# Performance work log

Measured on AMD Instinct MI355X. Metric: run time of the kernel, lower is better.

Reference implementation:

```python
import jax, jax.numpy as jnp
import numpy as np

MOMENTUM = 0.9
SHRINK = 0.0025
EPS_ATTN = 1e-8
EPS_NORM = 1e-12


def setup_inputs() -> dict:
    key = jax.random.key(0)
    ks = jax.random.split(key, 6)
    N, L, C, M = 64, 2048, 256, 128
    query = jax.random.normal(ks[0], (N, L, C), dtype=jnp.float32)
    mem = jax.random.normal(ks[1], (M, C), dtype=jnp.float32)
    # mimic xavier_normal + L2 row-normalize init
    mem = mem * np.sqrt(2.0 / (M + C))
    mem = mem / jnp.maximum(jnp.linalg.norm(mem, axis=1, keepdims=True), EPS_NORM)
    scale = 1.0 / np.sqrt(C)
    U_w = jax.random.uniform(ks[2], (C, C), jnp.float32, -scale, scale)
    U_b = jax.random.uniform(ks[3], (C,), jnp.float32, -scale, scale)
    W_w = jax.random.uniform(ks[4], (C, C), jnp.float32, -scale, scale)
    W_b = jax.random.uniform(ks[5], (C,), jnp.float32, -scale, scale)
    return {"query": query, "mem": mem, "U_w": U_w, "U_b": U_b, "W_w": W_w, "W_b": W_b}


def _hard_shrink_relu(x, lambd=SHRINK, epsilon=EPS_NORM):
    d = x - lambd
    return jax.nn.relu(d) * x / (jnp.abs(d) + epsilon)


def reference(query, mem, U_w, U_b, W_w, W_b):
    N, L, C = query.shape
    M = mem.shape[0]
    q = query.reshape(-1, C)  # T x C

    # ---- update (torch.no_grad block) ----
    qd = jax.lax.stop_gradient(q)
    m = jax.lax.stop_gradient(mem)
    attn_u = jax.nn.softmax(qd @ m.T, axis=-1)          # T x M
    attn_u = jnp.maximum(attn_u, EPS_ATTN)
    add_mem = attn_u.T @ qd                              # M x C
    gate = jax.nn.sigmoid(m @ U_w.T + U_b + add_mem @ W_w.T + W_b)
    new_mem = MOMENTUM * m + (1.0 - MOMENTUM) * ((1.0 - gate) * m + gate * add_mem)
    new_mem = new_mem / jnp.maximum(jnp.linalg.norm(new_mem, axis=1, keepdims=True), EPS_NORM)
    new_mem = jax.lax.stop_gradient(new_mem)

    # ---- read (memory detached, query differentiable) ----
    attn = jax.nn.softmax(q @ new_mem.T, axis=-1)        # T x M
    attn = _hard_shrink_relu(attn)
    attn = attn / jnp.maximum(jnp.sum(jnp.abs(attn), axis=1, keepdims=True), EPS_NORM)
    add_memory = attn @ new_mem                          # T x C
    out = jnp.concatenate([q, add_memory], axis=1)       # T x 2C

    out = out.reshape(N, L, 2 * C)
    attn = attn.reshape(N, L, M)
    return out, attn, new_mem
```

## Files before the change

### kernel.cpp

```cpp
#include <hip/hip_runtime.h>
#include <hip/hip_bf16.h>

#define T_TOT 131072

typedef __bf16 v8bf __attribute__((ext_vector_type(8)));
typedef float  v4f  __attribute__((ext_vector_type(4)));

#define MFMA16(a, b, c) __builtin_amdgcn_mfma_f32_16x16x32_bf16(a, b, c, 0, 0, 0)

__device__ __forceinline__ unsigned short f2bf(float x) {
  unsigned int u = __float_as_uint(x);
  u += 0x7fffu + ((u >> 16) & 1u);
  return (unsigned short)(u >> 16);
}
__device__ __forceinline__ ushort4 f2bf4(float4 v) {
  ushort4 r; r.x = f2bf(v.x); r.y = f2bf(v.y); r.z = f2bf(v.z); r.w = f2bf(v.w);
  return r;
}

__global__ void prep_kernel(const float* __restrict__ mem,
                            unsigned short* __restrict__ memb,
                            float* __restrict__ add_mem) {
  int i = blockIdx.x * 256 + threadIdx.x;
  memb[i] = f2bf(mem[i]);
  add_mem[i] = 0.f;
}

template <bool IS_READ>
__global__ __launch_bounds__(256, 2)
void attn_kernel(const float* __restrict__ q,
                 const unsigned short* __restrict__ memb,
                 unsigned short* __restrict__ attnT,
                 unsigned short* __restrict__ qbT,
                 float* __restrict__ attn_out,
                 const unsigned short* __restrict__ nmT,
                 float* __restrict__ out) {
  constexpr int R1 = 33792;
  __shared__ __align__(16) char smem[IS_READ ? (R1 + 17408) : R1];
  unsigned short* qs   = (unsigned short*)smem;
  unsigned short* ms   = (unsigned short*)(smem + 9216);
  float*          S    = (float*)smem;
  unsigned short* nmTl = (unsigned short*)smem;
  unsigned short* P    = (unsigned short*)(smem + R1);

  const int tid  = threadIdx.x;
  const int wave = tid >> 6, lane = tid & 63, l15 = lane & 15, quad = lane >> 4;
  const int t0 = blockIdx.x * 64;
  const int rh = wave >> 1, mh = wave & 1;

  v4f acc[2][4] = {};

  for (int kc = 0; kc < 256; kc += 64) {
    __syncthreads();
#pragma unroll
    for (int i = 0; i < 4; ++i) {
      int f4 = tid + i * 256, row = f4 >> 4, c4 = f4 & 15;
      float4 v = *(const float4*)(q + (size_t)(t0 + row) * 256 + kc + c4 * 4);
      if constexpr (IS_READ)
        *(float4*)(out + (size_t)(t0 + row) * 512 + kc + c4 * 4) = v;
      *(ushort4*)(qs + row * 72 + c4 * 4) = f2bf4(v);
    }
#pragma unroll
    for (int i = 0; i < 4; ++i) {
      int g = tid + i * 256, m = g >> 3, c8 = g & 7;
      *(uint4*)(ms + m * 72 + c8 * 8) = *(const uint4*)(memb + m * 256 + kc + c8 * 8);
    }
    __syncthreads();
#pragma unroll
    for (int s = 0; s < 2; ++s) {
      int ko = s * 32 + quad * 8;
      v8bf a0 = *(const v8bf*)(qs + (rh * 32 + l15) * 72 + ko);
      v8bf a1 = *(const v8bf*)(qs + (rh * 32 + 16 + l15) * 72 + ko);
#pragma unroll
      for (int j = 0; j < 4; ++j) {
        v8bf b = *(const v8bf*)(ms + (mh * 64 + j * 16 + l15) * 72 + ko);
        acc[0][j] = MFMA16(a0, b, acc[0][j]);
        acc[1][j] = MFMA16(a1, b, acc[1][j]);
      }
    }
    if constexpr (!IS_READ) {
      int c4 = tid & 63, g = tid >> 6;
      const unsigned short* qcol = qs + c4;
      unsigned int pk2[8];
#pragma unroll
      for (int j = 0; j < 8; ++j) {
        unsigned int lo = qcol[(g * 16 + j * 2) * 72];
        unsigned int hi = qcol[(g * 16 + j * 2 + 1) * 72];
        pk2[j] = lo | (hi << 16);
      }
      uint4* dq = (uint4*)(qbT + (size_t)(kc + c4) * T_TOT + t0 + g * 16);
      dq[0] = make_uint4(pk2[0], pk2[1], pk2[2], pk2[3]);
      dq[1] = make_uint4(pk2[4], pk2[5], pk2[6], pk2[7]);
    }
  }
  __syncthreads();
#pragma unroll
  for (int i = 0; i < 2; ++i)
#pragma unroll
    for (int j = 0; j < 4; ++j)
#pragma unroll
      for (int r = 0; r < 4; ++r)
        S[(rh * 32 + i * 16 + quad * 4 + r) * 132 + mh * 64 + j * 16 + l15] = acc[i][j][r];
  __syncthreads();

  const int row = tid >> 2, p = tid & 3;
  float4 v[8];
  float mx = -1e30f;
#pragma unroll
  for (int k = 0; k < 8; ++k) {
    v[k] = *(const float4*)(S + row * 132 + p * 32 + k * 4);
    mx = fmaxf(mx, fmaxf(fmaxf(v[k].x, v[k].y), fmaxf(v[k].z, v[k].w)));
  }
  mx = fmaxf(mx, __shfl_xor(mx, 1, 64));
  mx = fmaxf(mx, __shfl_xor(mx, 2, 64));
  float sum = 0.f;
#pragma unroll
  for (int k = 0; k < 8; ++k) {
    v[k].x = __expf(v[k].x - mx); v[k].y = __expf(v[k].y - mx);
    v[k].z = __expf(v[k].z - mx); v[k].w = __expf(v[k].w - mx);
    sum += v[k].x + v[k].y + v[k].z + v[k].w;
  }
  sum += __shfl_xor(sum, 1, 64);
  sum += __shfl_xor(sum, 2, 64);
  float inv = 1.f / sum;

  if constexpr (!IS_READ) {
#pragma unroll
    for (int k = 0; k < 8; ++k) {
      v[k].x = fmaxf(v[k].x * inv, 1e-8f); v[k].y = fmaxf(v[k].y * inv, 1e-8f);
      v[k].z = fmaxf(v[k].z * inv, 1e-8f); v[k].w = fmaxf(v[k].w * inv, 1e-8f);
      *(float4*)(S + row * 132 + p * 32 + k * 4) = v[k];
    }
    __syncthreads();
    int m = tid >> 1, hf = tid & 1;
    unsigned int pk[16];
#pragma unroll
    for (int k2 = 0; k2 < 16; ++k2) {
      unsigned int lo = f2bf(S[(hf * 32 + k2 * 2) * 132 + m]);
      unsigned int hi = f2bf(S[(hf * 32 + k2 * 2 + 1) * 132 + m]);
      pk[k2] = lo | (hi << 16);
    }
    uint4* dst = (uint4*)(attnT + (size_t)m * T_TOT + t0 + hf * 32);
    dst[0] = make_uint4(pk[0], pk[1], pk[2], pk[3]);
    dst[1] = make_uint4(pk[4], pk[5], pk[6], pk[7]);
    dst[2] = make_uint4(pk[8], pk[9], pk[10], pk[11]);
    dst[3] = make_uint4(pk[12], pk[13], pk[14], pk[15]);
  } else {
    float ysum = 0.f;
#pragma unroll
    for (int k = 0; k < 8; ++k) {
      float* e = (float*)&v[k];
#pragma unroll
      for (int c = 0; c < 4; ++c) {
        float a2 = e[c] * inv;
        float dd = a2 - 0.0025f;
        float y  = dd > 0.f ? a2 * dd / (dd + 1e-12f) : 0.f;
        e[c] = y; ysum += y;
      }
    }
    ysum += __shfl_xor(ysum, 1, 64);
    ysum += __shfl_xor(ysum, 2, 64);
    float dn = 1.f / fmaxf(ysum, 1e-12f);
#pragma unroll
    for (int k = 0; k < 8; ++k) {
      float4 w; w.x = v[k].x * dn; w.y = v[k].y * dn; w.z = v[k].z * dn; w.w = v[k].w * dn;
      *(float4*)(attn_out + (size_t)(t0 + row) * 128 + p * 32 + k * 4) = w;
      *(ushort4*)(P + row * 136 + p * 32 + k * 4) = f2bf4(w);
    }
    __syncthreads();

    v4f acc2[16] = {};
    for (int mc = 0; mc < 128; mc += 32) {
#pragma unroll
      for (int i = 0; i < 4; ++i) {
        int g = tid + i * 256, cr = g >> 2, c8 = g & 3;
        *(uint4*)(nmTl + cr * 56 + c8 * 8) = *(const uint4*)(nmT + cr * 128 + mc + c8 * 8);
      }
      __syncthreads();
      v8bf af = *(const v8bf*)(P + (wave * 16 + l15) * 136 + mc + quad * 8);
#pragma unroll
      for (int j2 = 0; j2 < 16; ++j2) {
        v8bf bf = *(const v8bf*)(nmTl + (j2 * 16 + l15) * 56 + quad * 8);
        acc2[j2] = MFMA16(af, bf, acc2[j2]);
      }
      __syncthreads();
    }
#pragma unroll
    for (int j2 = 0; j2 < 16; ++j2)
#pragma unroll
      for (int r = 0; r < 4; ++r)
        out[(size_t)(t0 + wave * 16 + quad * 4 + r) * 512 + 256 + j2 * 16 + l15] = acc2[j2][r];
  }
}

__global__ __launch_bounds__(256, 2)
void addmem_kernel(const unsigned short* __restrict__ attnT,
                   const unsigned short* __restrict__ qbT,
                   float* __restrict__ add_mem) {
  __shared__ __align__(16) char smem[36864];
  unsigned short* at_l = (unsigned short*)smem;
  unsigned short* qb_l = (unsigned short*)(smem + 18432);
  const int tid  = threadIdx.x;
  const int wave = tid >> 6, lane = tid & 63, l15 = lane & 15, quad = lane >> 4;
  const int h  = blockIdx.x & 1;
  const int tc = blockIdx.x >> 1;
  const int wm = wave & 1, wc = wave >> 1;
  v4f acc[4][4] = {};

  for (int kk = 0; kk < 8; ++kk) {
    int kb = tc * 512 + kk * 64;
    __syncthreads();
#pragma unroll
    for (int i = 0; i < 4; ++i) {
      int g = tid + i * 256, m = g >> 3, t8 = g & 7;
      *(uint4*)(at_l + m * 72 + t8 * 8) =
          *(const uint4*)(attnT + (size_t)m * T_TOT + kb + t8 * 8);
      *(uint4*)(qb_l + m * 72 + t8 * 8) =
          *(const uint4*)(qbT + (size_t)(h * 128 + m) * T_TOT + kb + t8 * 8);
    }
    __syncthreads();
#pragma unroll
    for (int s = 0; s < 2; ++s) {
      int ko = s * 32 + quad * 8;
      v8bf a[4], b[4];
#pragma unroll
      for (int jm = 0; jm < 4; ++jm)
        a[jm] = *(const v8bf*)(at_l + (wm * 64 + jm * 16 + l15) * 72 + ko);
#pragma unroll
      for (int jc = 0; jc < 4; ++jc)
        b[jc] = *(const v8bf*)(qb_l + (wc * 64 + jc * 16 + l15) * 72 + ko);
#pragma unroll
      for (int jm = 0; jm < 4; ++jm)
#pragma unroll
        for (int jc = 0; jc < 4; ++jc)
          acc[jm][jc] = MFMA16(a[jm], b[jc], acc[jm][jc]);
    }
  }
#pragma unroll
  for (int jm = 0; jm < 4; ++jm)
#pragma unroll
    for (int jc = 0; jc < 4; ++jc)
#pragma unroll
      for (int r = 0; r < 4; ++r)
        atomicAdd(add_mem + (wm * 64 + jm * 16 + quad * 4 + r) * 256 +
                      h * 128 + wc * 64 + jc * 16 + l15,
                  acc[jm][jc][r]);
}

__global__ __launch_bounds__(256)
void update_kernel(const float* __restrict__ mem, const float* __restrict__ add_mem,
                   const float* __restrict__ U_w, const float* __restrict__ U_b,
                   const float* __restrict__ W_w, const float* __restrict__ W_b,
                   float* __restrict__ nm_out, unsigned short* __restrict__ nm_bf,
                   unsigned short* __restrict__ nmT_bf) {
  const int m = blockIdx.x, c = threadIdx.x;
  __shared__ float mrow[256], arow[256], red[8];
  mrow[c] = mem[m * 256 + c];
  arow[c] = add_mem[m * 256 + c];
  __syncthreads();
  float g = U_b[c] + W_b[c];
  const float4* uw = (const float4*)(U_w + (size_t)c * 256);
  const float4* ww = (const float4*)(W_w + (size_t)c * 256);
#pragma unroll 8
  for (int k = 0; k < 64; ++k) {
    float4 u4 = uw[k], w4 = ww[k];
    g += u4.x * mrow[k * 4] + u4.y * mrow[k * 4 + 1] + u4.z * mrow[k * 4 + 2] + u4.w * mrow[k * 4 + 3];
    g += w4.x * arow[k * 4] + w4.y * arow[k * 4 + 1] + w4.z * arow[k * 4 + 2] + w4.w * arow[k * 4 + 3];
  }
  float gate = 1.f / (1.f + __expf(-g));
  float nmv = mrow[c] * (1.f - 0.1f * gate) + 0.1f * gate * arow[c];
  float ss = nmv * nmv;
#pragma unroll
  for (int o = 1; o < 64; o <<= 1) ss += __shfl_xor(ss, o, 64);
  int wv = c >> 6, lane = c & 63;
  if (lane == 0) red[wv] = ss;
  __syncthreads();
  if (c == 0) red[4] = 1.f / fmaxf(sqrtf(red[0] + red[1] + red[2] + red[3]), 1e-12f);
  __syncthreads();
  float nv = nmv * red[4];
  nm_out[m * 256 + c] = nv;
  unsigned short b = f2bf(nv);
  nm_bf[m * 256 + c] = b;
  nmT_bf[c * 128 + m] = b;
}

extern "C" void kernel_launch(void* const* d_in, const int* in_sizes, int n_in,
                              void* d_out, int out_size, void* d_ws, size_t ws_size,
                              hipStream_t stream) {
  (void)in_sizes; (void)n_in; (void)out_size; (void)ws_size;
  const float* q   = (const float*)d_in[0];
  const float* mem = (const float*)d_in[1];
  const float* U_w = (const float*)d_in[2];
  const float* U_b = (const float*)d_in[3];
  const float* W_w = (const float*)d_in[4];
  const float* W_b = (const float*)d_in[5];

  float* out      = (float*)d_out;
  float* attn_out = out + (size_t)T_TOT * 512;
  float* nm_out   = attn_out + (size_t)T_TOT * 128;

  float*          add_mem = (float*)d_ws;
  unsigned short* mem_bf  = (unsigned short*)((char*)d_ws + 131072);
  unsigned short* nm_bf   = (unsigned short*)((char*)d_ws + 196608);
  unsigned short* nmT_bf  = (unsigned short*)((char*)d_ws + 262144);
  unsigned short* attnT = (unsigned short*)attn_out;
  unsigned short* qbT   = (unsigned short*)out;

  prep_kernel<<<128, 256, 0, stream>>>(mem, mem_bf, add_mem);
  attn_kernel<false><<<2048, 256, 0, stream>>>(q, mem_bf, attnT, qbT, nullptr, nullptr, nullptr);
  addmem_kernel<<<512, 256, 0, stream>>>(attnT, qbT, add_mem);
  update_kernel<<<128, 256, 0, stream>>>(mem, add_mem, U_w, U_b, W_w, W_b,
                                         nm_out, nm_bf, nmT_bf);
  attn_kernel<true><<<2048, 256, 0, stream>>>(q, nm_bf, nullptr, nullptr, attn_out, nmT_bf, out);
}
```

Measured before the change: 569.7 us.

## Split attention kernel and load read-pass operands directly from global memory

The templated attention kernel is split into separate write and read kernels. The read kernel no longer stages query and memory tiles in LDS. Each lane loads its query fragment straight from global memory, converts it to bf16 in registers, and reads memory and the transposed new-memory B fragments directly from global (cache-resident) instead of through shared memory. This removes several __syncthreads and LDS round trips. In exchange it issues more redundant global/L2 loads per wave and uses less-coalesced access patterns.

```diff
diff --git a/kernel.cpp b/kernel.cpp
--- a/kernel.cpp
+++ b/kernel.cpp
@@ -16,6 +16,11 @@
 __device__ __forceinline__ ushort4 f2bf4(float4 v) {
   ushort4 r; r.x = f2bf(v.x); r.y = f2bf(v.y); r.z = f2bf(v.z); r.w = f2bf(v.w);
   return r;
+}
+__device__ __forceinline__ v8bf f2bf8(float4 lo, float4 hi) {
+  union { ushort4 u[2]; v8bf v; } r;
+  r.u[0] = f2bf4(lo); r.u[1] = f2bf4(hi);
+  return r.v;
 }
 
 __global__ void prep_kernel(const float* __restrict__ mem,
@@ -26,22 +31,15 @@
   add_mem[i] = 0.f;
 }
 
-template <bool IS_READ>
 __global__ __launch_bounds__(256, 2)
-void attn_kernel(const float* __restrict__ q,
-                 const unsigned short* __restrict__ memb,
-                 unsigned short* __restrict__ attnT,
-                 unsigned short* __restrict__ qbT,
-                 float* __restrict__ attn_out,
-                 const unsigned short* __restrict__ nmT,
-                 float* __restrict__ out) {
-  constexpr int R1 = 33792;
-  __shared__ __align__(16) char smem[IS_READ ? (R1 + 17408) : R1];
-  unsigned short* qs   = (unsigned short*)smem;
-  unsigned short* ms   = (unsigned short*)(smem + 9216);
-  float*          S    = (float*)smem;
-  unsigned short* nmTl = (unsigned short*)smem;
-  unsigned short* P    = (unsigned short*)(smem + R1);
+void attn_write_kernel(const float* __restrict__ q,
+                       const unsigned short* __restrict__ memb,
+                       unsigned short* __restrict__ attnT,
+                       unsigned short* __restrict__ qbT) {
+  __shared__ __align__(16) char smem[33792];
+  unsigned short* qs = (unsigned short*)smem;
+  unsigned short* ms = (unsigned short*)(smem + 9216);
+  float*          S  = (float*)smem;
 
   const int tid  = threadIdx.x;
   const int wave = tid >> 6, lane = tid & 63, l15 = lane & 15, quad = lane >> 4;
@@ -56,8 +54,6 @@
     for (int i = 0; i < 4; ++i) {
       int f4 = tid + i * 256, row = f4 >> 4, c4 = f4 & 15;
       float4 v = *(const float4*)(q + (size_t)(t0 + row) * 256 + kc + c4 * 4);
-      if constexpr (IS_READ)
-        *(float4*)(out + (size_t)(t0 + row) * 512 + kc + c4 * 4) = v;
       *(ushort4*)(qs + row * 72 + c4 * 4) = f2bf4(v);
     }
 #pragma unroll
@@ -78,7 +74,7 @@
         acc[1][j] = MFMA16(a1, b, acc[1][j]);
       }
     }
-    if constexpr (!IS_READ) {
+    {
       int c4 = tid & 63, g = tid >> 6;
       const unsigned short* qcol = qs + c4;
       unsigned int pk2[8];
@@ -124,73 +120,135 @@
   sum += __shfl_xor(sum, 2, 64);
   float inv = 1.f / sum;
 
-  if constexpr (!IS_READ) {
-#pragma unroll
-    for (int k = 0; k < 8; ++k) {
-      v[k].x = fmaxf(v[k].x * inv, 1e-8f); v[k].y = fmaxf(v[k].y * inv, 1e-8f);
-      v[k].z = fmaxf(v[k].z * inv, 1e-8f); v[k].w = fmaxf(v[k].w * inv, 1e-8f);
-      *(float4*)(S + row * 132 + p * 32 + k * 4) = v[k];
-    }
-    __syncthreads();
-    int m = tid >> 1, hf = tid & 1;
-    unsigned int pk[16];
-#pragma unroll
-    for (int k2 = 0; k2 < 16; ++k2) {
-      unsigned int lo = f2bf(S[(hf * 32 + k2 * 2) * 132 + m]);
-      unsigned int hi = f2bf(S[(hf * 32 + k2 * 2 + 1) * 132 + m]);
-      pk[k2] = lo | (hi << 16);
-    }
-    uint4* dst = (uint4*)(attnT + (size_t)m * T_TOT + t0 + hf * 32);
-    dst[0] = make_uint4(pk[0], pk[1], pk[2], pk[3]);
-    dst[1] = make_uint4(pk[4], pk[5], pk[6], pk[7]);
-    dst[2] = make_uint4(pk[8], pk[9], pk[10], pk[11]);
-    dst[3] = make_uint4(pk[12], pk[13], pk[14], pk[15]);
-  } else {
-    float ysum = 0.f;
-#pragma unroll
-    for (int k = 0; k < 8; ++k) {
-      float* e = (float*)&v[k];
-#pragma unroll
-      for (int c = 0; c < 4; ++c) {
-        float a2 = e[c] * inv;
-        float dd = a2 - 0.0025f;
-        float y  = dd > 0.f ? a2 * dd / (dd + 1e-12f) : 0.f;
-        e[c] = y; ysum += y;
-      }
-    }
-    ysum += __shfl_xor(ysum, 1, 64);
-    ysum += __shfl_xor(ysum, 2, 64);
-    float dn = 1.f / fmaxf(ysum, 1e-12f);
-#pragma unroll
-    for (int k = 0; k < 8; ++k) {
-      float4 w; w.x = v[k].x * dn; w.y = v[k].y * dn; w.z = v[k].z * dn; w.w = v[k].w * dn;
-      *(float4*)(attn_out + (size_t)(t0 + row) * 128 + p * 32 + k * 4) = w;
-      *(ushort4*)(P + row * 136 + p * 32 + k * 4) = f2bf4(w);
-    }
-    __syncthreads();
-
-    v4f acc2[16] = {};
-    for (int mc = 0; mc < 128; mc += 32) {
-#pragma unroll
-      for (int i = 0; i < 4; ++i) {
-        int g = tid + i * 256, cr = g >> 2, c8 = g & 3;
-        *(uint4*)(nmTl + cr * 56 + c8 * 8) = *(const uint4*)(nmT + cr * 128 + mc + c8 * 8);
-      }
-      __syncthreads();
-      v8bf af = *(const v8bf*)(P + (wave * 16 + l15) * 136 + mc + quad * 8);
-#pragma unroll
-      for (int j2 = 0; j2 < 16; ++j2) {
-        v8bf bf = *(const v8bf*)(nmTl + (j2 * 16 + l15) * 56 + quad * 8);
-        acc2[j2] = MFMA16(af, bf, acc2[j2]);
-      }
-      __syncthreads();
-    }
-#pragma unroll
-    for (int j2 = 0; j2 < 16; ++j2)
+#pragma unroll
+  for (int k = 0; k < 8; ++k) {
+    v[k].x = fmaxf(v[k].x * inv, 1e-8f); v[k].y = fmaxf(v[k].y * inv, 1e-8f);
+    v[k].z = fmaxf(v[k].z * inv, 1e-8f); v[k].w = fmaxf(v[k].w * inv, 1e-8f);
+    *(float4*)(S + row * 132 + p * 32 + k * 4) = v[k];
+  }
+  __syncthreads();
+  int m = tid >> 1, hf = tid & 1;
+  unsigned int pk[16];
+#pragma unroll
+  for (int k2 = 0; k2 < 16; ++k2) {
+    unsigned int lo = f2bf(S[(hf * 32 + k2 * 2) * 132 + m]);
+    unsigned int hi = f2bf(S[(hf * 32 + k2 * 2 + 1) * 132 + m]);
+    pk[k2] = lo | (hi << 16);
+  }
+  uint4* dst = (uint4*)(attnT + (size_t)m * T_TOT + t0 + hf * 32);
+  dst[0] = make_uint4(pk[0], pk[1], pk[2], pk[3]);
+  dst[1] = make_uint4(pk[4], pk[5], pk[6], pk[7]);
+  dst[2] = make_uint4(pk[8], pk[9], pk[10], pk[11]);
+  dst[3] = make_uint4(pk[12], pk[13], pk[14], pk[15]);
+}
+
+__global__ __launch_bounds__(256, 2)
+void attn_read_kernel(const float* __restrict__ q,
+                      const unsigned short* __restrict__ memb,
+                      float* __restrict__ attn_out,
+                      const unsigned short* __restrict__ nmT,
+                      float* __restrict__ out) {
+  __shared__ __align__(16) char smem[51200];
+  float*          S = (float*)smem;
+  unsigned short* P = (unsigned short*)(smem + 33792);
+
+  const int tid  = threadIdx.x;
+  const int wave = tid >> 6, lane = tid & 63, l15 = lane & 15, quad = lane >> 4;
+  const int t0 = blockIdx.x * 64;
+  const int rh = wave >> 1, mh = wave & 1;
+  const int r0 = t0 + rh * 32 + l15;
+  const int r1 = r0 + 16;
+
+  v4f acc[2][4] = {};
+#pragma unroll
+  for (int s8 = 0; s8 < 8; ++s8) {
+    int ko = s8 * 32 + quad * 8;
+    float4 a0lo = *(const float4*)(q + (size_t)r0 * 256 + ko);
+    float4 a0hi = *(const float4*)(q + (size_t)r0 * 256 + ko + 4);
+    float4 a1lo = *(const float4*)(q + (size_t)r1 * 256 + ko);
+    float4 a1hi = *(const float4*)(q + (size_t)r1 * 256 + ko + 4);
+    if (mh == 0) {
+      *(float4*)(out + (size_t)r0 * 512 + ko)     = a0lo;
+      *(float4*)(out + (size_t)r0 * 512 + ko + 4) = a0hi;
+      *(float4*)(out + (size_t)r1 * 512 + ko)     = a1lo;
+      *(float4*)(out + (size_t)r1 * 512 + ko + 4) = a1hi;
+    }
+    v8bf a0 = f2bf8(a0lo, a0hi);
+    v8bf a1 = f2bf8(a1lo, a1hi);
+#pragma unroll
+    for (int j = 0; j < 4; ++j) {
+      v8bf b = *(const v8bf*)(memb + (size_t)(mh * 64 + j * 16 + l15) * 256 + ko);
+      acc[0][j] = MFMA16(a0, b, acc[0][j]);
+      acc[1][j] = MFMA16(a1, b, acc[1][j]);
+    }
+  }
+#pragma unroll
+  for (int i = 0; i < 2; ++i)
+#pragma unroll
+    for (int j = 0; j < 4; ++j)
 #pragma unroll
       for (int r = 0; r < 4; ++r)
-        out[(size_t)(t0 + wave * 16 + quad * 4 + r) * 512 + 256 + j2 * 16 + l15] = acc2[j2][r];
-  }
+        S[(rh * 32 + i * 16 + quad * 4 + r) * 132 + mh * 64 + j * 16 + l15] = acc[i][j][r];
+  __syncthreads();
+
+  const int row = tid >> 2, p = tid & 3;
+  float4 v[8];
+  float mx = -1e30f;
+#pragma unroll
+  for (int k = 0; k < 8; ++k) {
+    v[k] = *(const float4*)(S + row * 132 + p * 32 + k * 4);
+    mx = fmaxf(mx, fmaxf(fmaxf(v[k].x, v[k].y), fmaxf(v[k].z, v[k].w)));
+  }
+  mx = fmaxf(mx, __shfl_xor(mx, 1, 64));
+  mx = fmaxf(mx, __shfl_xor(mx, 2, 64));
+  float sum = 0.f;
+#pragma unroll
+  for (int k = 0; k < 8; ++k) {
+    v[k].x = __expf(v[k].x - mx); v[k].y = __expf(v[k].y - mx);
+    v[k].z = __expf(v[k].z - mx); v[k].w = __expf(v[k].w - mx);
+    sum += v[k].x + v[k].y + v[k].z + v[k].w;
+  }
+  sum += __shfl_xor(sum, 1, 64);
+  sum += __shfl_xor(sum, 2, 64);
+  float inv = 1.f / sum;
+
+  float ysum = 0.f;
+#pragma unroll
+  for (int k = 0; k < 8; ++k) {
+    float* e = (float*)&v[k];
+#pragma unroll
+    for (int c = 0; c < 4; ++c) {
+      float a2 = e[c] * inv;
+      float dd = a2 - 0.0025f;
+      float y  = dd > 0.f ? a2 * dd / (dd + 1e-12f) : 0.f;
+      e[c] = y; ysum += y;
+    }
+  }
+  ysum += __shfl_xor(ysum, 1, 64);
+  ysum += __shfl_xor(ysum, 2, 64);
+  float dn = 1.f / fmaxf(ysum, 1e-12f);
+#pragma unroll
+  for (int k = 0; k < 8; ++k) {
+    float4 w; w.x = v[k].x * dn; w.y = v[k].y * dn; w.z = v[k].z * dn; w.w = v[k].w * dn;
+    *(float4*)(attn_out + (size_t)(t0 + row) * 128 + p * 32 + k * 4) = w;
+    *(ushort4*)(P + row * 136 + p * 32 + k * 4) = f2bf4(w);
+  }
+
+  v4f acc2[16] = {};
+#pragma unroll
+  for (int mc = 0; mc < 128; mc += 32) {
+    v8bf af = *(const v8bf*)(P + (wave * 16 + l15) * 136 + mc + quad * 8);
+#pragma unroll
+    for (int j2 = 0; j2 < 16; ++j2) {
+      v8bf bf = *(const v8bf*)(nmT + (size_t)(j2 * 16 + l15) * 128 + mc + quad * 8);
+      acc2[j2] = MFMA16(af, bf, acc2[j2]);
+    }
+  }
+#pragma unroll
+  for (int j2 = 0; j2 < 16; ++j2)
+#pragma unroll
+    for (int r = 0; r < 4; ++r)
+      out[(size_t)(t0 + wave * 16 + quad * 4 + r) * 512 + 256 + j2 * 16 + l15] = acc2[j2][r];
 }
 
 __global__ __launch_bounds__(256, 2)
@@ -307,9 +365,9 @@
   unsigned short* qbT   = (unsigned short*)out;
 
   prep_kernel<<<128, 256, 0, stream>>>(mem, mem_bf, add_mem);
-  attn_kernel<false><<<2048, 256, 0, stream>>>(q, mem_bf, attnT, qbT, nullptr, nullptr, nullptr);
+  attn_write_kernel<<<2048, 256, 0, stream>>>(q, mem_bf, attnT, qbT);
   addmem_kernel<<<512, 256, 0, stream>>>(attnT, qbT, add_mem);
   update_kernel<<<128, 256, 0, stream>>>(mem, add_mem, U_w, U_b, W_w, W_b,
                                          nm_out, nm_bf, nmT_bf);
-  attn_kernel<true><<<2048, 256, 0, stream>>>(q, nm_bf, nullptr, nullptr, attn_out, nmT_bf, out);
-}
+  attn_read_kernel<<<2048, 256, 0, stream>>>(q, nm_bf, attn_out, nmT_bf, out);
+}
```

Result: slower. 649.9 us (+14.1%).

## Replace atomic add_mem accumulation with partial buffers plus a reduce kernel

Applied to the files above, without the earlier changes.

The addmem kernel now writes per-block partial M×C/2 tiles into scratch space in the output buffer instead of using float atomicAdd into add_mem. A new reduce kernel sums the 256 partials per half, and the zeroing of add_mem in prep is dropped. The update-phase attn kernel also gets a launch bound of 3 blocks per CU to raise occupancy. This trades atomic contention for about 32 MB of extra partial-buffer traffic and one more kernel launch. The reduce runs only 128 blocks, which may underuse the GPU.

```diff
diff --git a/kernel.cpp b/kernel.cpp
--- a/kernel.cpp
+++ b/kernel.cpp
@@ -19,15 +19,13 @@
 }
 
 __global__ void prep_kernel(const float* __restrict__ mem,
-                            unsigned short* __restrict__ memb,
-                            float* __restrict__ add_mem) {
+                            unsigned short* __restrict__ memb) {
   int i = blockIdx.x * 256 + threadIdx.x;
   memb[i] = f2bf(mem[i]);
-  add_mem[i] = 0.f;
 }
 
 template <bool IS_READ>
-__global__ __launch_bounds__(256, 2)
+__global__ __launch_bounds__(256, IS_READ ? 2 : 3)
 void attn_kernel(const float* __restrict__ q,
                  const unsigned short* __restrict__ memb,
                  unsigned short* __restrict__ attnT,
@@ -196,7 +194,7 @@
 __global__ __launch_bounds__(256, 2)
 void addmem_kernel(const unsigned short* __restrict__ attnT,
                    const unsigned short* __restrict__ qbT,
-                   float* __restrict__ add_mem) {
+                   float* __restrict__ part) {
   __shared__ __align__(16) char smem[36864];
   unsigned short* at_l = (unsigned short*)smem;
   unsigned short* qb_l = (unsigned short*)(smem + 18432);
@@ -236,15 +234,32 @@
           acc[jm][jc] = MFMA16(a[jm], b[jc], acc[jm][jc]);
     }
   }
+  float* pt = part + ((size_t)h * 256 + tc) * 16384;
 #pragma unroll
   for (int jm = 0; jm < 4; ++jm)
 #pragma unroll
     for (int jc = 0; jc < 4; ++jc)
 #pragma unroll
       for (int r = 0; r < 4; ++r)
-        atomicAdd(add_mem + (wm * 64 + jm * 16 + quad * 4 + r) * 256 +
-                      h * 128 + wc * 64 + jc * 16 + l15,
-                  acc[jm][jc][r]);
+        pt[(wm * 64 + jm * 16 + quad * 4 + r) * 128 + wc * 64 + jc * 16 + l15] =
+            acc[jm][jc][r];
+}
+
+__global__ __launch_bounds__(256)
+void reduce_kernel(const float* __restrict__ part,
+                   float* __restrict__ add_mem) {
+  int g = blockIdx.x * 256 + threadIdx.x;
+  int h = g >> 14, e = g & 16383;
+  const float* p = part + (size_t)h * 256 * 16384 + e;
+  float s0 = 0.f, s1 = 0.f, s2 = 0.f, s3 = 0.f;
+  for (int k = 0; k < 256; k += 4) {
+    s0 += p[(size_t)(k + 0) * 16384];
+    s1 += p[(size_t)(k + 1) * 16384];
+    s2 += p[(size_t)(k + 2) * 16384];
+    s3 += p[(size_t)(k + 3) * 16384];
+  }
+  int m = e >> 7, cl = e & 127;
+  add_mem[m * 256 + h * 128 + cl] = (s0 + s1) + (s2 + s3);
 }
 
 __global__ __launch_bounds__(256)
@@ -305,10 +320,12 @@
   unsigned short* nmT_bf  = (unsigned short*)((char*)d_ws + 262144);
   unsigned short* attnT = (unsigned short*)attn_out;
   unsigned short* qbT   = (unsigned short*)out;
-
-  prep_kernel<<<128, 256, 0, stream>>>(mem, mem_bf, add_mem);
+  float*          part  = out + (size_t)40 * 1024 * 1024;
+
+  prep_kernel<<<128, 256, 0, stream>>>(mem, mem_bf);
   attn_kernel<false><<<2048, 256, 0, stream>>>(q, mem_bf, attnT, qbT, nullptr, nullptr, nullptr);
-  addmem_kernel<<<512, 256, 0, stream>>>(attnT, qbT, add_mem);
+  addmem_kernel<<<512, 256, 0, stream>>>(attnT, qbT, part);
+  reduce_kernel<<<128, 256, 0, stream>>>(part, add_mem);
   update_kernel<<<128, 256, 0, stream>>>(mem, add_mem, U_w, U_b, W_w, W_b,
                                          nm_out, nm_bf, nmT_bf);
   attn_kernel<true><<<2048, 256, 0, stream>>>(q, nm_bf, nullptr, nullptr, attn_out, nmT_bf, out);
```

New measurement: 564.5 us. Within noise of the previous version (-0.9%).
